# Kernel tuning notes

Measured on AMD Instinct MI355X. Metric: run time of the kernel, lower is better.

Reference implementation:

```python
import jax, jax.numpy as jnp
import numpy as np

DIM = 1024
HEADS = 16
DIM_HEAD = 64
INNER = HEADS * DIM_HEAD  # 1024
P = INNER  # num_param_tokens
B, N = 4, 2048
LN_EPS = 1e-5
NORM_EPS = 1e-12


def _pattention(x, key_tok, val_tok):
    # x: [..., dim_in]; key_tok: [P, dim_in]; val_tok: [P, dim_out]
    scale = key_tok.shape[1] ** (-0.5)
    sim = jnp.einsum('bnd,pd->bnp', x, key_tok) * scale
    # F.normalize(p=2, dim=-1) with eps=1e-12
    nrm = jnp.maximum(jnp.linalg.norm(sim, axis=-1, keepdims=True), NORM_EPS)
    attn = jax.nn.gelu(sim / nrm, approximate=False)  # torch F.gelu default = exact erf
    return jnp.einsum('bnp,pe->bne', attn, val_tok)


def setup_inputs() -> dict:
    key = jax.random.key(0)
    ks = jax.random.split(key, 11)
    d = {
        'x': jax.random.normal(ks[0], (B, N, DIM), dtype=jnp.float32),
        'ln_gamma': jnp.ones((DIM,), dtype=jnp.float32),
        'ln_beta': jnp.zeros((DIM,), dtype=jnp.float32),
        'q_key': jax.random.normal(ks[1], (P, DIM), dtype=jnp.float32),
        'q_val': jax.random.normal(ks[2], (P, INNER), dtype=jnp.float32),
        'k_key': jax.random.normal(ks[3], (P, DIM), dtype=jnp.float32),
        'k_val': jax.random.normal(ks[4], (P, INNER), dtype=jnp.float32),
        'v_key': jax.random.normal(ks[5], (P, DIM), dtype=jnp.float32),
        'v_val': jax.random.normal(ks[6], (P, INNER), dtype=jnp.float32),
        'o_key': jax.random.normal(ks[7], (P, INNER), dtype=jnp.float32),
        'o_val': jax.random.normal(ks[8], (P, DIM), dtype=jnp.float32),
    }
    return d


def reference(x, ln_gamma, ln_beta, q_key, q_val, k_key, k_val, v_key, v_val, o_key, o_val):
    # LayerNorm (torch default: elementwise affine, eps=1e-5)
    mu = jnp.mean(x, axis=-1, keepdims=True)
    var = jnp.mean(jnp.square(x - mu), axis=-1, keepdims=True)
    x_norm = (x - mu) / jnp.sqrt(var + LN_EPS) * ln_gamma + ln_beta

    q = _pattention(x_norm, q_key, q_val)  # [B, N, INNER]
    k = _pattention(x_norm, k_key, k_val)
    v = _pattention(x_norm, v_key, v_val)

    # b n (h d) -> b h n d
    def split_heads(t):
        return t.reshape(B, N, HEADS, DIM_HEAD).transpose(0, 2, 1, 3)

    q, k, v = split_heads(q), split_heads(k), split_heads(v)
    scale = DIM_HEAD ** (-0.5)
    dots = jnp.einsum('bhnd,bhmd->bhnm', q, k) * scale  # [B, H, N, N]
    attn = jax.nn.softmax(dots, axis=-1)  # dropout p=0 -> identity
    out = jnp.einsum('bhnm,bhmd->bhnd', attn, v)
    out = out.transpose(0, 2, 1, 3).reshape(B, N, INNER)  # b h n d -> b n (h d)
    return _pattention(out, o_key, o_val)
```

## Files before the change

### kernel.cpp

```cpp
#include <hip/hip_runtime.h>
#include <hip/hip_bf16.h>
#include <stdint.h>

#define DIMSZ 1024
#define BN_TOT 8192
#define NSEQ 2048
#define NHEADS 16
#define DHEAD 64

typedef __attribute__((ext_vector_type(8))) __bf16 bf16x8;
typedef __attribute__((ext_vector_type(4))) float f32x4;

__device__ __forceinline__ float bf2f(ushort u) {
  return __uint_as_float(((uint32_t)u) << 16);
}
__device__ __forceinline__ ushort f2bf(float f) {
  uint32_t u = __float_as_uint(f);
  u += 0x7FFFu + ((u >> 16) & 1u);
  return (ushort)(u >> 16);
}
__device__ __forceinline__ uint32_t cvt_pk_bf16(float lo, float hi) {
  uint32_t r;
  asm("v_cvt_pk_bf16_f32 %0, %1, %2" : "=v"(r) : "v"(lo), "v"(hi));
  return r;
}
__device__ __forceinline__ void gl_lds16(const ushort* g, ushort* l) {
  __builtin_amdgcn_global_load_lds(
      (const __attribute__((address_space(1))) void*)g,
      (__attribute__((address_space(3))) void*)l, 16, 0, 0);
}

__global__ __launch_bounds__(256) void layernorm_k(
    const float* __restrict__ x, const float* __restrict__ gamma,
    const float* __restrict__ beta, ushort* __restrict__ xn) {
  const int row = blockIdx.x;
  const int tid = threadIdx.x;
  const float* xr = x + (size_t)row * DIMSZ;
  float4 v = *(const float4*)(xr + tid * 4);
  float s = v.x + v.y + v.z + v.w;
  float ss = v.x * v.x + v.y * v.y + v.z * v.z + v.w * v.w;
#pragma unroll
  for (int o = 1; o < 64; o <<= 1) { s += __shfl_xor(s, o); ss += __shfl_xor(ss, o); }
  __shared__ float red[2][4];
  const int wid = tid >> 6;
  if ((tid & 63) == 0) { red[0][wid] = s; red[1][wid] = ss; }
  __syncthreads();
  s = red[0][0] + red[0][1] + red[0][2] + red[0][3];
  ss = red[1][0] + red[1][1] + red[1][2] + red[1][3];
  const float mu = s * (1.0f / DIMSZ);
  const float var = ss * (1.0f / DIMSZ) - mu * mu;
  const float rstd = rsqrtf(var + 1e-5f);
  float4 g = *(const float4*)(gamma + tid * 4);
  float4 bb = *(const float4*)(beta + tid * 4);
  ushort4 o4;
  o4.x = f2bf((v.x - mu) * rstd * g.x + bb.x);
  o4.y = f2bf((v.y - mu) * rstd * g.y + bb.y);
  o4.z = f2bf((v.z - mu) * rstd * g.z + bb.z);
  o4.w = f2bf((v.w - mu) * rstd * g.w + bb.w);
  *(ushort4*)(xn + (size_t)row * DIMSZ + tid * 4) = o4;
}

__global__ __launch_bounds__(256) void normgelu_k(
    const float* __restrict__ sim, ushort* __restrict__ out) {
  const int row = blockIdx.x;
  const int tid = threadIdx.x;
  const float* sr = sim + (size_t)row * DIMSZ;
  float4 v = *(const float4*)(sr + tid * 4);
  float ss = v.x * v.x + v.y * v.y + v.z * v.z + v.w * v.w;
#pragma unroll
  for (int o = 1; o < 64; o <<= 1) ss += __shfl_xor(ss, o);
  __shared__ float red[4];
  if ((tid & 63) == 0) red[tid >> 6] = ss;
  __syncthreads();
  ss = red[0] + red[1] + red[2] + red[3];
  const float inv = 1.0f / fmaxf(sqrtf(ss), 1e-12f);
  ushort4 o4;
  float x0;
  x0 = v.x * inv; o4.x = f2bf(0.5f * x0 * (1.0f + erff(x0 * 0.70710678118654752f)));
  x0 = v.y * inv; o4.y = f2bf(0.5f * x0 * (1.0f + erff(x0 * 0.70710678118654752f)));
  x0 = v.z * inv; o4.z = f2bf(0.5f * x0 * (1.0f + erff(x0 * 0.70710678118654752f)));
  x0 = v.w * inv; o4.w = f2bf(0.5f * x0 * (1.0f + erff(x0 * 0.70710678118654752f)));
  *(ushort4*)(out + (size_t)row * DIMSZ + tid * 4) = o4;
}

__global__ void cvt_k(const float* __restrict__ in, ushort* __restrict__ out, int n) {
  int i = (blockIdx.x * 256 + threadIdx.x) * 4;
  if (i < n) {
    float4 v = *(const float4*)(in + i);
    ushort4 o;
    o.x = f2bf(v.x); o.y = f2bf(v.y); o.z = f2bf(v.z); o.w = f2bf(v.w);
    *(ushort4*)(out + i) = o;
  }
}

__global__ __launch_bounds__(256) void transpose_cvt_k(
    const float* __restrict__ in, ushort* __restrict__ out) {
  __shared__ float t[32][33];
  const int tx = threadIdx.x & 31;
  const int ty = threadIdx.x >> 5;
  const int bx = blockIdx.x * 32;
  const int by = blockIdx.y * 32;
#pragma unroll
  for (int i = 0; i < 32; i += 8)
    t[ty + i][tx] = in[(size_t)(by + ty + i) * DIMSZ + bx + tx];
  __syncthreads();
#pragma unroll
  for (int i = 0; i < 32; i += 8)
    out[(size_t)(bx + ty + i) * DIMSZ + by + tx] = f2bf(t[tx][ty + i]);
}

__global__ __launch_bounds__(256) void transpose_v_k(
    const ushort* __restrict__ vb, ushort* __restrict__ vt) {
  __shared__ ushort t[32][33];
  const int bh = blockIdx.x;
  const int nt = blockIdx.y;
  const int dt = blockIdx.z;
  const int b = bh >> 4, h = bh & 15;
  const int tx = threadIdx.x & 31;
  const int ty = threadIdx.x >> 5;
  const size_t inbase = ((size_t)b * NSEQ + nt * 32) * DIMSZ + h * DHEAD + dt * 32;
#pragma unroll
  for (int i = 0; i < 32; i += 8)
    t[ty + i][tx] = vb[inbase + (size_t)(ty + i) * DIMSZ + tx];
  __syncthreads();
  const size_t outbase = ((size_t)bh * DHEAD + dt * 32) * NSEQ + nt * 32;
#pragma unroll
  for (int i = 0; i < 32; i += 8)
    vt[outbase + (size_t)(ty + i) * NSEQ + tx] = t[tx][ty + i];
}

template <int OUT_BF16>
__global__ __launch_bounds__(256) void gemm_nt_k(
    const ushort* __restrict__ A, const ushort* __restrict__ B,
    void* __restrict__ Cout, int M, int N, int K) {
  __shared__ ushort As[3][128 * 32];
  __shared__ ushort Bs[3][128 * 32];
  const int tid = threadIdx.x;
  const int lane = tid & 63;
  const int wid = tid >> 6;
  const int i0 = blockIdx.x * 128;
  const int n0 = blockIdx.y * 128;
  const int wr = (wid >> 1) * 64;
  const int wc = (wid & 1) * 64;
  f32x4 acc[4][4];
#pragma unroll
  for (int m = 0; m < 4; ++m)
#pragma unroll
    for (int n = 0; n < 4; ++n) acc[m][n] = (f32x4){0.f, 0.f, 0.f, 0.f};
  const int fr = lane & 15;
  const int g = lane >> 4;
  const int kg = (g ^ ((fr >> 1) & 3)) * 8;
  const int srow = wid * 32 + (lane >> 2);
  const int skc = ((lane & 3) ^ ((lane >> 3) & 3)) * 8;
  const ushort* Ag = A + (size_t)(i0 + srow) * K + skc;
  const ushort* Bg = B + (size_t)(n0 + srow) * K + skc;
  const int wb = wid * 1024;

#define STAGE_TILE(tt, bb)                                      \
  do {                                                          \
    gl_lds16(Ag + (tt) * 32, &As[bb][wb]);                      \
    gl_lds16(Ag + (size_t)16 * K + (tt) * 32, &As[bb][wb + 512]); \
    gl_lds16(Bg + (tt) * 32, &Bs[bb][wb]);                      \
    gl_lds16(Bg + (size_t)16 * K + (tt) * 32, &Bs[bb][wb + 512]); \
  } while (0)

  const int nt = K >> 5;
  STAGE_TILE(0, 0);
  STAGE_TILE(1, 1);
  asm volatile("s_waitcnt vmcnt(4)" ::: "memory");
  __builtin_amdgcn_s_barrier();

  int cur = 0;
  for (int t = 0; t < nt; ++t) {
    if (t + 2 < nt) {
      const int nb = (cur >= 1) ? cur - 1 : cur + 2;
      STAGE_TILE(t + 2, nb);
    }
    bf16x8 af[4], bfr[4];
#pragma unroll
    for (int m = 0; m < 4; ++m)
      af[m] = *(const bf16x8*)&As[cur][(wr + m * 16 + fr) * 32 + kg];
#pragma unroll
    for (int n = 0; n < 4; ++n)
      bfr[n] = *(const bf16x8*)&Bs[cur][(wc + n * 16 + fr) * 32 + kg];
#pragma unroll
    for (int m = 0; m < 4; ++m)
#pragma unroll
      for (int n = 0; n < 4; ++n)
        acc[m][n] = __builtin_amdgcn_mfma_f32_16x16x32_bf16(af[m], bfr[n], acc[m][n], 0, 0, 0);
    if (t + 2 < nt)
      asm volatile("s_waitcnt vmcnt(4)" ::: "memory");
    else
      asm volatile("s_waitcnt vmcnt(0)" ::: "memory");
    __builtin_amdgcn_s_barrier();
    cur = (cur == 2) ? 0 : cur + 1;
  }
#undef STAGE_TILE

  const int rq = lane >> 4;
#pragma unroll
  for (int m = 0; m < 4; ++m) {
#pragma unroll
    for (int n = 0; n < 4; ++n) {
#pragma unroll
      for (int rr = 0; rr < 4; ++rr) {
        const int row = i0 + wr + m * 16 + rq * 4 + rr;
        const int col = n0 + wc + n * 16 + fr;
        if (OUT_BF16)
          ((ushort*)Cout)[(size_t)row * N + col] = f2bf(acc[m][n][rr]);
        else
          ((float*)Cout)[(size_t)row * N + col] = acc[m][n][rr];
      }
    }
  }
}

__global__ __launch_bounds__(256, 4) void flash_mfma_k(
    const ushort* __restrict__ Qm, const ushort* __restrict__ Km,
    const ushort* __restrict__ Vt, ushort* __restrict__ Om) {
  __shared__ ushort Ks[64 * 72];
  __shared__ ushort Vs[64 * 72];
  __shared__ ushort Ps[4][32 * 72];
  const int tid = threadIdx.x;
  const int lane = tid & 63;
  const int wid = tid >> 6;
  const int bh = blockIdx.x;
  const int qb = blockIdx.y;
  const int bidx = bh >> 4;
  const int h = bh & 15;
  const size_t rowbase = (size_t)bidx * NSEQ;
  const int colbase = h * DHEAD;
  const int fr = lane & 15;
  const int g = lane >> 4;
  const int kg = g * 8;
  const int q0 = qb * 128 + wid * 32;

  bf16x8 qf[2][2];
#pragma unroll
  for (int m = 0; m < 2; ++m)
#pragma unroll
    for (int ks = 0; ks < 2; ++ks)
      qf[m][ks] = *(const bf16x8*)(Qm + (rowbase + q0 + m * 16 + fr) * (size_t)DIMSZ +
                                   colbase + ks * 32 + kg);

  f32x4 oaccT[2][4];
#pragma unroll
  for (int m = 0; m < 2; ++m)
#pragma unroll
    for (int n = 0; n < 4; ++n) oaccT[m][n] = (f32x4){0.f, 0.f, 0.f, 0.f};
  float m2[2] = {-1e30f, -1e30f};
  float l_run[2] = {0.f, 0.f};
  const float c1 = 0.125f * 1.44269504088896340736f;

  const ushort* Kg = Km + rowbase * DIMSZ + colbase;
  const ushort* Vg = Vt + (size_t)bh * DHEAD * NSEQ;
  const int sr = tid >> 3;
  const int c8 = (tid & 7) * 8;

  uint4 k0 = *(const uint4*)(Kg + (size_t)sr * DIMSZ + c8);
  uint4 k1 = *(const uint4*)(Kg + (size_t)(sr + 32) * DIMSZ + c8);
  uint4 v0 = *(const uint4*)(Vg + (size_t)sr * NSEQ + c8);
  uint4 v1 = *(const uint4*)(Vg + (size_t)(sr + 32) * NSEQ + c8);

  for (int kt = 0; kt < NSEQ / 64; ++kt) {
    __syncthreads();
    *(uint4*)&Ks[sr * 72 + c8] = k0;
    *(uint4*)&Ks[(sr + 32) * 72 + c8] = k1;
    *(uint4*)&Vs[sr * 72 + c8] = v0;
    *(uint4*)&Vs[(sr + 32) * 72 + c8] = v1;
    __syncthreads();
    if (kt + 1 < NSEQ / 64) {
      k0 = *(const uint4*)(Kg + (size_t)((kt + 1) * 64 + sr) * DIMSZ + c8);
      k1 = *(const uint4*)(Kg + (size_t)((kt + 1) * 64 + sr + 32) * DIMSZ + c8);
      v0 = *(const uint4*)(Vg + (size_t)sr * NSEQ + (kt + 1) * 64 + c8);
      v1 = *(const uint4*)(Vg + (size_t)(sr + 32) * NSEQ + (kt + 1) * 64 + c8);
    }

    f32x4 s[2][4];
#pragma unroll
    for (int m = 0; m < 2; ++m)
#pragma unroll
      for (int n = 0; n < 4; ++n) s[m][n] = (f32x4){0.f, 0.f, 0.f, 0.f};
    __builtin_amdgcn_s_setprio(1);
#pragma unroll
    for (int ks = 0; ks < 2; ++ks) {
      bf16x8 ak[4];
#pragma unroll
      for (int n = 0; n < 4; ++n)
        ak[n] = *(const bf16x8*)&Ks[(n * 16 + fr) * 72 + ks * 32 + kg];
#pragma unroll
      for (int m = 0; m < 2; ++m)
#pragma unroll
        for (int n = 0; n < 4; ++n)
          s[m][n] = __builtin_amdgcn_mfma_f32_16x16x32_bf16(ak[n], qf[m][ks], s[m][n], 0, 0, 0);
    }
    __builtin_amdgcn_s_setprio(0);

#pragma unroll
    for (int m = 0; m < 2; ++m) {
      float tm = fmaxf(fmaxf(fmaxf(s[m][0][0], s[m][0][1]), fmaxf(s[m][0][2], s[m][0][3])),
                       fmaxf(fmaxf(s[m][1][0], s[m][1][1]), fmaxf(s[m][1][2], s[m][1][3])));
      tm = fmaxf(tm,
                 fmaxf(fmaxf(fmaxf(s[m][2][0], s[m][2][1]), fmaxf(s[m][2][2], s[m][2][3])),
                       fmaxf(fmaxf(s[m][3][0], s[m][3][1]), fmaxf(s[m][3][2], s[m][3][3]))));
      tm = fmaxf(tm, __shfl_xor(tm, 16));
      tm = fmaxf(tm, __shfl_xor(tm, 32));
      const float tm2 = tm * c1;
      if (!__all(tm2 <= m2[m] + 8.0f)) {
        const float mn2 = fmaxf(m2[m], tm2);
        const float al = exp2f(m2[m] - mn2);
        l_run[m] *= al;
        m2[m] = mn2;
#pragma unroll
        for (int n = 0; n < 4; ++n) oaccT[m][n] *= al;
      }
      const float mref = m2[m];
      float p[4][4];
#pragma unroll
      for (int n = 0; n < 4; ++n)
#pragma unroll
        for (int rr = 0; rr < 4; ++rr) {
          p[n][rr] = exp2f(fmaf(s[m][n][rr], c1, -mref));
          s[m][n][rr] = p[n][rr];
        }
      const float t0 = (p[0][0] + p[0][1]) + (p[0][2] + p[0][3]);
      const float t1 = (p[1][0] + p[1][1]) + (p[1][2] + p[1][3]);
      const float t2 = (p[2][0] + p[2][1]) + (p[2][2] + p[2][3]);
      const float t3 = (p[3][0] + p[3][1]) + (p[3][2] + p[3][3]);
      float ps = (t0 + t1) + (t2 + t3);
      ps += __shfl_xor(ps, 16);
      ps += __shfl_xor(ps, 32);
      l_run[m] += ps;
    }

    ushort* pw = &Ps[wid][0];
#pragma unroll
    for (int m = 0; m < 2; ++m)
#pragma unroll
      for (int n = 0; n < 4; ++n) {
        uint2 w;
        w.x = cvt_pk_bf16(s[m][n][0], s[m][n][1]);
        w.y = cvt_pk_bf16(s[m][n][2], s[m][n][3]);
        *(uint2*)&pw[(m * 16 + fr) * 72 + n * 16 + g * 4] = w;
      }

    __builtin_amdgcn_s_setprio(1);
#pragma unroll
    for (int ks = 0; ks < 2; ++ks) {
      bf16x8 av[4], pb[2];
#pragma unroll
      for (int nd = 0; nd < 4; ++nd)
        av[nd] = *(const bf16x8*)&Vs[(nd * 16 + fr) * 72 + ks * 32 + kg];
#pragma unroll
      for (int m = 0; m < 2; ++m)
        pb[m] = *(const bf16x8*)&Ps[wid][(m * 16 + fr) * 72 + ks * 32 + kg];
#pragma unroll
      for (int m = 0; m < 2; ++m)
#pragma unroll
        for (int nd = 0; nd < 4; ++nd)
          oaccT[m][nd] = __builtin_amdgcn_mfma_f32_16x16x32_bf16(av[nd], pb[m], oaccT[m][nd], 0, 0, 0);
    }
    __builtin_amdgcn_s_setprio(0);
  }

#pragma unroll
  for (int m = 0; m < 2; ++m) {
    const float invl = 1.0f / l_run[m];
    const size_t row = rowbase + q0 + m * 16 + fr;
#pragma unroll
    for (int nd = 0; nd < 4; ++nd) {
      uint2 w;
      w.x = cvt_pk_bf16(oaccT[m][nd][0] * invl, oaccT[m][nd][1] * invl);
      w.y = cvt_pk_bf16(oaccT[m][nd][2] * invl, oaccT[m][nd][3] * invl);
      *(uint2*)(Om + row * DIMSZ + colbase + nd * 16 + g * 4) = w;
    }
  }
}

extern "C" void kernel_launch(void* const* d_in, const int* in_sizes, int n_in,
                              void* d_out, int out_size, void* d_ws, size_t ws_size,
                              hipStream_t stream) {
  (void)in_sizes; (void)n_in; (void)out_size; (void)ws_size;
  const float* x     = (const float*)d_in[0];
  const float* ln_g  = (const float*)d_in[1];
  const float* ln_b  = (const float*)d_in[2];
  const float* q_key = (const float*)d_in[3];
  const float* q_val = (const float*)d_in[4];
  const float* k_key = (const float*)d_in[5];
  const float* k_val = (const float*)d_in[6];
  const float* v_key = (const float*)d_in[7];
  const float* v_val = (const float*)d_in[8];
  const float* o_key = (const float*)d_in[9];
  const float* o_val = (const float*)d_in[10];
  float* out = (float*)d_out;

  char* ws = (char*)d_ws;
  const size_t MB = 1024 * 1024;
  ushort* xn    = (ushort*)(ws + 0 * MB);
  ushort* wkey  = (ushort*)(ws + 16 * MB);
  ushort* wvalT = (ushort*)(ws + 24 * MB);
  ushort* gelu  = (ushort*)(ws + 32 * MB);
  ushort* qb    = (ushort*)(ws + 48 * MB);
  ushort* kb    = (ushort*)(ws + 64 * MB);
  ushort* vb    = (ushort*)(ws + 80 * MB);
  ushort* aout  = (ushort*)(ws + 96 * MB);
  ushort* vt    = gelu;
  float* sim = (float*)d_out;

  const int NW = DIMSZ * DIMSZ;

  layernorm_k<<<BN_TOT, 256, 0, stream>>>(x, ln_g, ln_b, xn);
  cvt_k<<<1024, 256, 0, stream>>>(q_key, wkey + 0 * (size_t)NW, NW);
  cvt_k<<<1024, 256, 0, stream>>>(k_key, wkey + 1 * (size_t)NW, NW);
  cvt_k<<<1024, 256, 0, stream>>>(v_key, wkey + 2 * (size_t)NW, NW);
  cvt_k<<<1024, 256, 0, stream>>>(o_key, wkey + 3 * (size_t)NW, NW);
  dim3 tg(32, 32);
  transpose_cvt_k<<<tg, 256, 0, stream>>>(q_val, wvalT + 0 * (size_t)NW);
  transpose_cvt_k<<<tg, 256, 0, stream>>>(k_val, wvalT + 1 * (size_t)NW);
  transpose_cvt_k<<<tg, 256, 0, stream>>>(v_val, wvalT + 2 * (size_t)NW);
  transpose_cvt_k<<<tg, 256, 0, stream>>>(o_val, wvalT + 3 * (size_t)NW);

  dim3 gg(BN_TOT / 128, DIMSZ / 128);
  ushort* outs[3] = {qb, kb, vb};
  for (int t = 0; t < 3; ++t) {
    gemm_nt_k<0><<<gg, 256, 0, stream>>>(xn, wkey + t * (size_t)NW, sim, BN_TOT, DIMSZ, DIMSZ);
    normgelu_k<<<BN_TOT, 256, 0, stream>>>(sim, gelu);
    gemm_nt_k<1><<<gg, 256, 0, stream>>>(gelu, wvalT + t * (size_t)NW, outs[t], BN_TOT, DIMSZ, DIMSZ);
  }
  transpose_v_k<<<dim3(64, 64, 2), 256, 0, stream>>>(vb, vt);
  flash_mfma_k<<<dim3(64, 16), 256, 0, stream>>>(qb, kb, vt, aout);
  gemm_nt_k<0><<<gg, 256, 0, stream>>>(aout, wkey + 3 * (size_t)NW, sim, BN_TOT, DIMSZ, DIMSZ);
  normgelu_k<<<BN_TOT, 256, 0, stream>>>(sim, gelu);
  gemm_nt_k<0><<<gg, 256, 0, stream>>>(gelu, wvalT + 3 * (size_t)NW, (void*)out, BN_TOT, DIMSZ, DIMSZ);
}
```

Before: 434.3 us.

## Enlarge GEMM tile to 256x128 and compute softmax row sums via MFMA

The NT GEMM now uses 512-thread blocks covering 256x128 output tiles, with 8 waves sharing each B tile, to improve operand reuse and reduce global loads per FLOP. In the flash kernel, the per-row probability sum is computed by an extra MFMA against a row of ones appended to the V tile, replacing the scalar adds and cross-lane shuffles. The max reduction is also restructured. Fewer GEMM blocks (256) may leave some CUs idle or reduce latency hiding, and the extra MFMA adds matrix work per tile.

```diff
diff --git a/kernel.cpp b/kernel.cpp
--- a/kernel.cpp
+++ b/kernel.cpp
@@ -130,15 +130,15 @@
 }
 
 template <int OUT_BF16>
-__global__ __launch_bounds__(256) void gemm_nt_k(
+__global__ __launch_bounds__(512) void gemm_nt_k(
     const ushort* __restrict__ A, const ushort* __restrict__ B,
     void* __restrict__ Cout, int M, int N, int K) {
-  __shared__ ushort As[3][128 * 32];
+  __shared__ ushort As[3][256 * 32];
   __shared__ ushort Bs[3][128 * 32];
   const int tid = threadIdx.x;
   const int lane = tid & 63;
   const int wid = tid >> 6;
-  const int i0 = blockIdx.x * 128;
+  const int i0 = blockIdx.x * 256;
   const int n0 = blockIdx.y * 128;
   const int wr = (wid >> 1) * 64;
   const int wc = (wid & 1) * 64;
@@ -150,24 +150,25 @@
   const int fr = lane & 15;
   const int g = lane >> 4;
   const int kg = (g ^ ((fr >> 1) & 3)) * 8;
-  const int srow = wid * 32 + (lane >> 2);
+  const int srA = wid * 32 + (lane >> 2);
+  const int srB = wid * 16 + (lane >> 2);
   const int skc = ((lane & 3) ^ ((lane >> 3) & 3)) * 8;
-  const ushort* Ag = A + (size_t)(i0 + srow) * K + skc;
-  const ushort* Bg = B + (size_t)(n0 + srow) * K + skc;
-  const int wb = wid * 1024;
-
-#define STAGE_TILE(tt, bb)                                      \
-  do {                                                          \
-    gl_lds16(Ag + (tt) * 32, &As[bb][wb]);                      \
-    gl_lds16(Ag + (size_t)16 * K + (tt) * 32, &As[bb][wb + 512]); \
-    gl_lds16(Bg + (tt) * 32, &Bs[bb][wb]);                      \
-    gl_lds16(Bg + (size_t)16 * K + (tt) * 32, &Bs[bb][wb + 512]); \
+  const ushort* Ag = A + (size_t)(i0 + srA) * K + skc;
+  const ushort* Bg = B + (size_t)(n0 + srB) * K + skc;
+  const int wbA = wid * 1024;
+  const int wbB = wid * 512;
+
+#define STAGE_TILE(tt, bb)                                        \
+  do {                                                            \
+    gl_lds16(Ag + (tt) * 32, &As[bb][wbA]);                       \
+    gl_lds16(Ag + (size_t)16 * K + (tt) * 32, &As[bb][wbA + 512]); \
+    gl_lds16(Bg + (tt) * 32, &Bs[bb][wbB]);                       \
   } while (0)
 
   const int nt = K >> 5;
   STAGE_TILE(0, 0);
   STAGE_TILE(1, 1);
-  asm volatile("s_waitcnt vmcnt(4)" ::: "memory");
+  asm volatile("s_waitcnt vmcnt(3)" ::: "memory");
   __builtin_amdgcn_s_barrier();
 
   int cur = 0;
@@ -189,7 +190,7 @@
       for (int n = 0; n < 4; ++n)
         acc[m][n] = __builtin_amdgcn_mfma_f32_16x16x32_bf16(af[m], bfr[n], acc[m][n], 0, 0, 0);
     if (t + 2 < nt)
-      asm volatile("s_waitcnt vmcnt(4)" ::: "memory");
+      asm volatile("s_waitcnt vmcnt(3)" ::: "memory");
     else
       asm volatile("s_waitcnt vmcnt(0)" ::: "memory");
     __builtin_amdgcn_s_barrier();
@@ -219,7 +220,7 @@
     const ushort* __restrict__ Qm, const ushort* __restrict__ Km,
     const ushort* __restrict__ Vt, ushort* __restrict__ Om) {
   __shared__ ushort Ks[64 * 72];
-  __shared__ ushort Vs[64 * 72];
+  __shared__ ushort Vs[65 * 72];
   __shared__ ushort Ps[4][32 * 72];
   const int tid = threadIdx.x;
   const int lane = tid & 63;
@@ -235,6 +236,8 @@
   const int kg = g * 8;
   const int q0 = qb * 128 + wid * 32;
 
+  if (tid < 64) Vs[64 * 72 + tid] = 0x3F80;
+
   bf16x8 qf[2][2];
 #pragma unroll
   for (int m = 0; m < 2; ++m)
@@ -244,12 +247,14 @@
                                    colbase + ks * 32 + kg);
 
   f32x4 oaccT[2][4];
-#pragma unroll
-  for (int m = 0; m < 2; ++m)
+  f32x4 lacc[2];
+#pragma unroll
+  for (int m = 0; m < 2; ++m) {
 #pragma unroll
     for (int n = 0; n < 4; ++n) oaccT[m][n] = (f32x4){0.f, 0.f, 0.f, 0.f};
+    lacc[m] = (f32x4){0.f, 0.f, 0.f, 0.f};
+  }
   float m2[2] = {-1e30f, -1e30f};
-  float l_run[2] = {0.f, 0.f};
   const float c1 = 0.125f * 1.44269504088896340736f;
 
   const ushort* Kg = Km + rowbase * DIMSZ + colbase;
@@ -298,39 +303,31 @@
 
 #pragma unroll
     for (int m = 0; m < 2; ++m) {
-      float tm = fmaxf(fmaxf(fmaxf(s[m][0][0], s[m][0][1]), fmaxf(s[m][0][2], s[m][0][3])),
-                       fmaxf(fmaxf(s[m][1][0], s[m][1][1]), fmaxf(s[m][1][2], s[m][1][3])));
-      tm = fmaxf(tm,
-                 fmaxf(fmaxf(fmaxf(s[m][2][0], s[m][2][1]), fmaxf(s[m][2][2], s[m][2][3])),
-                       fmaxf(fmaxf(s[m][3][0], s[m][3][1]), fmaxf(s[m][3][2], s[m][3][3]))));
+      const float a0 = fmaxf(fmaxf(s[m][0][0], s[m][0][1]), s[m][0][2]);
+      const float a1 = fmaxf(fmaxf(s[m][0][3], s[m][1][0]), s[m][1][1]);
+      const float a2 = fmaxf(fmaxf(s[m][1][2], s[m][1][3]), s[m][2][0]);
+      const float a3 = fmaxf(fmaxf(s[m][2][1], s[m][2][2]), s[m][2][3]);
+      const float a4 = fmaxf(fmaxf(s[m][3][0], s[m][3][1]), s[m][3][2]);
+      const float b0 = fmaxf(fmaxf(a0, a1), a2);
+      const float b1 = fmaxf(fmaxf(a3, a4), s[m][3][3]);
+      float tm = fmaxf(b0, b1);
       tm = fmaxf(tm, __shfl_xor(tm, 16));
       tm = fmaxf(tm, __shfl_xor(tm, 32));
       const float tm2 = tm * c1;
       if (!__all(tm2 <= m2[m] + 8.0f)) {
         const float mn2 = fmaxf(m2[m], tm2);
         const float al = exp2f(m2[m] - mn2);
-        l_run[m] *= al;
         m2[m] = mn2;
+        lacc[m] *= al;
 #pragma unroll
         for (int n = 0; n < 4; ++n) oaccT[m][n] *= al;
       }
       const float mref = m2[m];
-      float p[4][4];
 #pragma unroll
       for (int n = 0; n < 4; ++n)
 #pragma unroll
-        for (int rr = 0; rr < 4; ++rr) {
-          p[n][rr] = exp2f(fmaf(s[m][n][rr], c1, -mref));
-          s[m][n][rr] = p[n][rr];
-        }
-      const float t0 = (p[0][0] + p[0][1]) + (p[0][2] + p[0][3]);
-      const float t1 = (p[1][0] + p[1][1]) + (p[1][2] + p[1][3]);
-      const float t2 = (p[2][0] + p[2][1]) + (p[2][2] + p[2][3]);
-      const float t3 = (p[3][0] + p[3][1]) + (p[3][2] + p[3][3]);
-      float ps = (t0 + t1) + (t2 + t3);
-      ps += __shfl_xor(ps, 16);
-      ps += __shfl_xor(ps, 32);
-      l_run[m] += ps;
+        for (int rr = 0; rr < 4; ++rr)
+          s[m][n][rr] = exp2f(fmaf(s[m][n][rr], c1, -mref));
     }
 
     ushort* pw = &Ps[wid][0];
@@ -348,6 +345,7 @@
 #pragma unroll
     for (int ks = 0; ks < 2; ++ks) {
       bf16x8 av[4], pb[2];
+      const bf16x8 av1 = *(const bf16x8*)&Vs[64 * 72 + ks * 32 + kg];
 #pragma unroll
       for (int nd = 0; nd < 4; ++nd)
         av[nd] = *(const bf16x8*)&Vs[(nd * 16 + fr) * 72 + ks * 32 + kg];
@@ -355,17 +353,19 @@
       for (int m = 0; m < 2; ++m)
         pb[m] = *(const bf16x8*)&Ps[wid][(m * 16 + fr) * 72 + ks * 32 + kg];
 #pragma unroll
-      for (int m = 0; m < 2; ++m)
+      for (int m = 0; m < 2; ++m) {
 #pragma unroll
         for (int nd = 0; nd < 4; ++nd)
           oaccT[m][nd] = __builtin_amdgcn_mfma_f32_16x16x32_bf16(av[nd], pb[m], oaccT[m][nd], 0, 0, 0);
+        lacc[m] = __builtin_amdgcn_mfma_f32_16x16x32_bf16(av1, pb[m], lacc[m], 0, 0, 0);
+      }
     }
     __builtin_amdgcn_s_setprio(0);
   }
 
 #pragma unroll
   for (int m = 0; m < 2; ++m) {
-    const float invl = 1.0f / l_run[m];
+    const float invl = 1.0f / lacc[m][0];
     const size_t row = rowbase + q0 + m * 16 + fr;
 #pragma unroll
     for (int nd = 0; nd < 4; ++nd) {
@@ -420,16 +420,16 @@
   transpose_cvt_k<<<tg, 256, 0, stream>>>(v_val, wvalT + 2 * (size_t)NW);
   transpose_cvt_k<<<tg, 256, 0, stream>>>(o_val, wvalT + 3 * (size_t)NW);
 
-  dim3 gg(BN_TOT / 128, DIMSZ / 128);
+  dim3 gg(BN_TOT / 256, DIMSZ / 128);
   ushort* outs[3] = {qb, kb, vb};
   for (int t = 0; t < 3; ++t) {
-    gemm_nt_k<0><<<gg, 256, 0, stream>>>(xn, wkey + t * (size_t)NW, sim, BN_TOT, DIMSZ, DIMSZ);
+    gemm_nt_k<0><<<gg, 512, 0, stream>>>(xn, wkey + t * (size_t)NW, sim, BN_TOT, DIMSZ, DIMSZ);
     normgelu_k<<<BN_TOT, 256, 0, stream>>>(sim, gelu);
-    gemm_nt_k<1><<<gg, 256, 0, stream>>>(gelu, wvalT + t * (size_t)NW, outs[t], BN_TOT, DIMSZ, DIMSZ);
+    gemm_nt_k<1><<<gg, 512, 0, stream>>>(gelu, wvalT + t * (size_t)NW, outs[t], BN_TOT, DIMSZ, DIMSZ);
   }
   transpose_v_k<<<dim3(64, 64, 2), 256, 0, stream>>>(vb, vt);
   flash_mfma_k<<<dim3(64, 16), 256, 0, stream>>>(qb, kb, vt, aout);
-  gemm_nt_k<0><<<gg, 256, 0, stream>>>(aout, wkey + 3 * (size_t)NW, sim, BN_TOT, DIMSZ, DIMSZ);
+  gemm_nt_k<0><<<gg, 512, 0, stream>>>(aout, wkey + 3 * (size_t)NW, sim, BN_TOT, DIMSZ, DIMSZ);
   normgelu_k<<<BN_TOT, 256, 0, stream>>>(sim, gelu);
-  gemm_nt_k<0><<<gg, 256, 0, stream>>>(gelu, wvalT + 3 * (size_t)NW, (void*)out, BN_TOT, DIMSZ, DIMSZ);
-}
+  gemm_nt_k<0><<<gg, 512, 0, stream>>>(gelu, wvalT + 3 * (size_t)NW, (void*)out, BN_TOT, DIMSZ, DIMSZ);
+}
```

After: 557.2 us. +28.3%, slower.
